# Performance work log

Measured on AMD Instinct MI355X. Metric: run time of the kernel, lower is better.

## Reference

```python
import jax, jax.numpy as jnp
import numpy as np


def setup_inputs() -> dict:
    key = jax.random.key(0)
    ks = jax.random.split(key, 8)
    C, dk = 256, 32
    B, H, W = 4, 64, 64
    x = jax.random.normal(ks[0], (B, C, H, W), dtype=jnp.float32)
    wq = jax.random.normal(ks[1], (dk, C), dtype=jnp.float32) * (1.0 / np.sqrt(C))
    bq = jnp.zeros((dk,), dtype=jnp.float32)
    wk = jax.random.normal(ks[2], (dk, C), dtype=jnp.float32) * (1.0 / np.sqrt(C))
    bk = jnp.zeros((dk,), dtype=jnp.float32)
    wv = jax.random.normal(ks[3], (C, C), dtype=jnp.float32) * (1.0 / np.sqrt(C))
    bv = jnp.zeros((C,), dtype=jnp.float32)
    gamma = jnp.ones((1,), dtype=jnp.float32)
    return {"x": x, "wq": wq, "bq": bq, "wk": wk, "bk": bk,
            "wv": wv, "bv": bv, "gamma": gamma}


def reference(x, wq, bq, wk, bk, wv, bv, gamma):
    B, C, H, W = x.shape
    N = H * W
    xf = x.reshape(B, C, N)  # [B, C, N]
    # 1x1 convs == per-pixel linear projections
    q = jnp.einsum('dc,bcn->bnd', wq, xf) + bq  # [B, N, dk]  (proj_query, permuted)
    k = jnp.einsum('dc,bcn->bdn', wk, xf) + bk[None, :, None]  # [B, dk, N]
    v = jnp.einsum('ec,bcn->ben', wv, xf) + bv[None, :, None]  # [B, C, N]
    energy = jnp.einsum('bnd,bdm->bnm', q, k)  # [B, N, N]
    attention = jax.nn.softmax(energy, axis=-1)
    # out[b,c,i] = sum_j v[b,c,j] * attention[b,i,j]
    out = jnp.einsum('bcj,bij->bci', v, attention)  # [B, C, N]
    out = out.reshape(B, C, H, W)
    return gamma[0] * out + x
```

## Files before the change

kernel.cpp:

```cpp
#include <hip/hip_runtime.h>
#include <hip/hip_bf16.h>

#define NPIX 4096
#define CIN  256
#define DK   32

typedef __attribute__((ext_vector_type(8))) short short8;
typedef __attribute__((ext_vector_type(16))) float f32x16;

__device__ __forceinline__ unsigned short f2bf(float f) {
    unsigned int u = __float_as_uint(f);
    return (unsigned short)((u + 0x7fffu + ((u >> 16) & 1u)) >> 16);
}
__device__ __forceinline__ float bf2f(unsigned short h) {
    return __uint_as_float(((unsigned int)h) << 16);
}
__device__ __forceinline__ unsigned int f2bf2(float a, float b) {
    __hip_bfloat162 h = __float22bfloat162_rn(make_float2(a, b));
    unsigned int u;
    __builtin_memcpy(&u, &h, 4);
    return u;
}

__global__ void wprep_kernel(const float* __restrict__ wq, const float* __restrict__ wk,
                             const float* __restrict__ wv,
                             unsigned short* __restrict__ wqh, unsigned short* __restrict__ wql,
                             unsigned short* __restrict__ wkh, unsigned short* __restrict__ wkl,
                             unsigned short* __restrict__ wvh) {
    const int lane = threadIdx.x & 63, li = lane & 31, hi = lane >> 5;
    const int kc = blockIdx.x, y = blockIdx.y;
    if (y < 4) {
        const float* m = (y < 2) ? wq : wk;
        short8 h8, l8;
#pragma unroll
        for (int e = 0; e < 8; ++e) {
            float v = m[li * CIN + kc * 16 + hi * 8 + e];
            unsigned short hb = f2bf(v);
            h8[e] = (short)hb;
            l8[e] = (short)f2bf(v - bf2f(hb));
        }
        unsigned short* dst = (y == 0) ? wqh : (y == 1) ? wql : (y == 2) ? wkh : wkl;
        *reinterpret_cast<short8*>(&dst[kc * 512 + lane * 8]) = (y & 1) ? l8 : h8;
    } else {
        const int cblk = y - 4;
        short8 h8;
#pragma unroll
        for (int e = 0; e < 8; ++e)
            h8[e] = (short)f2bf(wv[(cblk * 32 + li) * CIN + kc * 16 + hi * 8 + e]);
        *reinterpret_cast<short8*>(&wvh[(cblk * 16 + kc) * 512 + lane * 8]) = h8;
    }
}

__global__ __launch_bounds__(512) void projall_kernel(
        const float* __restrict__ x,
        const unsigned short* __restrict__ wqh, const unsigned short* __restrict__ wql,
        const unsigned short* __restrict__ wkh, const unsigned short* __restrict__ wkl,
        const unsigned short* __restrict__ wvh,
        const float* __restrict__ bq, const float* __restrict__ bk, const float* __restrict__ bv,
        unsigned short* __restrict__ qfrag, unsigned short* __restrict__ kfrag,
        unsigned short* __restrict__ vfrag) {
    __shared__ float xs[64][36];
    __shared__ unsigned short xhf[16 * 512];
    __shared__ unsigned short xlf[16 * 512];
    __shared__ unsigned short ts[2][32][40];

    const int t = threadIdx.x, lane = t & 63, li = lane & 31, hi = lane >> 5, w = t >> 6;
    const int nblk = blockIdx.x, b = blockIdx.y;
    const int n0 = nblk * 32;

    for (int cb = 0; cb < 4; ++cb) {
        {
            int c = t >> 3, n4 = (t & 7) * 4;
            float4 v = *reinterpret_cast<const float4*>(
                &x[(size_t)(b * CIN + cb * 64 + c) * NPIX + n0 + n4]);
            xs[c][n4 + 0] = v.x; xs[c][n4 + 1] = v.y;
            xs[c][n4 + 2] = v.z; xs[c][n4 + 3] = v.w;
        }
        __syncthreads();
        {
            const int kc = w & 3;
            const bool isL = (w >= 4);
            short8 f;
#pragma unroll
            for (int e = 0; e < 8; ++e) {
                float v = xs[kc * 16 + hi * 8 + e][li];
                unsigned short hb = f2bf(v);
                f[e] = isL ? (short)f2bf(v - bf2f(hb)) : (short)hb;
            }
            unsigned short* dst = isL ? xlf : xhf;
            *reinterpret_cast<short8*>(&dst[(cb * 4 + kc) * 512 + lane * 8]) = f;
        }
        __syncthreads();
    }

    if (w < 2) {
        const unsigned short* wh = (w == 0) ? wqh : wkh;
        const unsigned short* wl = (w == 0) ? wql : wkl;
        const float* bias = (w == 0) ? bq : bk;
        f32x16 acc;
#pragma unroll
        for (int r = 0; r < 16; ++r) acc[r] = 0.f;
        for (int kc = 0; kc < 16; ++kc) {
            short8 ah = *reinterpret_cast<const short8*>(&xhf[kc * 512 + lane * 8]);
            short8 al = *reinterpret_cast<const short8*>(&xlf[kc * 512 + lane * 8]);
            short8 whf = *reinterpret_cast<const short8*>(&wh[kc * 512 + lane * 8]);
            short8 wlf = *reinterpret_cast<const short8*>(&wl[kc * 512 + lane * 8]);
            acc = __builtin_amdgcn_mfma_f32_32x32x16_bf16(ah, whf, acc, 0, 0, 0);
            acc = __builtin_amdgcn_mfma_f32_32x32x16_bf16(al, whf, acc, 0, 0, 0);
            acc = __builtin_amdgcn_mfma_f32_32x32x16_bf16(ah, wlf, acc, 0, 0, 0);
        }
        const float bs = bias[li];
#pragma unroll
        for (int r = 0; r < 16; ++r) {
            int row = (r & 3) + 8 * (r >> 2) + 4 * hi;
            ts[w][row][li] = f2bf(acc[r] + bs);
        }
        unsigned short* dstf = (w == 0) ? qfrag : kfrag;
#pragma unroll
        for (int dh = 0; dh < 2; ++dh) {
            short8 f = *reinterpret_cast<const short8*>(&ts[w][li][dh * 16 + hi * 8]);
            *reinterpret_cast<short8*>(
                &dstf[((size_t)(b * 128 + nblk) * 2 + dh) * 512 + lane * 8]) = f;
        }
    } else {
        const int w2 = w - 2;
        const int njob = (w2 < 2) ? 2 : 1;
        for (int jj = 0; jj < njob; ++jj) {
            const int cblk = w2 + jj * 6;
            f32x16 acc;
#pragma unroll
            for (int r = 0; r < 16; ++r) acc[r] = 0.f;
            for (int kc = 0; kc < 16; ++kc) {
                short8 xb = *reinterpret_cast<const short8*>(&xhf[kc * 512 + lane * 8]);
                short8 wf = *reinterpret_cast<const short8*>(&wvh[(cblk * 16 + kc) * 512 + lane * 8]);
                acc = __builtin_amdgcn_mfma_f32_32x32x16_bf16(xb, wf, acc, 0, 0, 0);
            }
            const float bvv = bv[cblk * 32 + li];
#pragma unroll
            for (int g = 0; g < 2; ++g) {
                short8 sv;
#pragma unroll
                for (int e = 0; e < 8; ++e) sv[e] = (short)f2bf(acc[g * 8 + e] + bvv);
                *reinterpret_cast<short8*>(
                    &vfrag[((size_t)(b * 8 + cblk) * 256 + nblk * 2 + g) * 512 + lane * 8]) = sv;
            }
        }
    }
}

__global__ __launch_bounds__(512, 4) void attnv_kernel(
        const unsigned short* __restrict__ qfrag, const unsigned short* __restrict__ kfrag,
        const unsigned short* __restrict__ vfrag, unsigned short* __restrict__ opart,
        float* __restrict__ lpart, float* __restrict__ out) {
    __shared__ unsigned short Ps[4 * 8 * 512];
    __shared__ float sred[2][4][32];

    const int t = threadIdx.x, lane = t & 63, li = lane & 31, hi = lane >> 5, w = t >> 6;
    const int blk = blockIdx.x;
    const int xcd = blk & 7, slot = blk >> 3;
    const int jh = slot & 1, ps = slot >> 1;
    const int b = xcd >> 1;
    const int ipos = (xcd & 1) * 32 + ps;
    const int it = w >> 2, sl = w & 3;
    const int cq = w;

    short8 qb0, qb1;
    {
        size_t qoff = ((size_t)(b * 128 + ipos * 2 + it) * 2) * 512 + lane * 8;
        qb0 = *reinterpret_cast<const short8*>(&qfrag[qoff]);
        qb1 = *reinterpret_cast<const short8*>(&qfrag[qoff + 512]);
    }
    float ssum = 0.f;

    f32x16 acc0, acc1;
#pragma unroll
    for (int r = 0; r < 16; ++r) { acc0[r] = 0.f; acc1[r] = 0.f; }

    short8 kp0, kp1;
    short8 vp[8];

    auto kload = [&](int s) {
        size_t koff = ((size_t)(b * 128 + jh * 64 + s * 4 + sl) * 2) * 512 + lane * 8;
        kp0 = *reinterpret_cast<const short8*>(&kfrag[koff]);
        kp1 = *reinterpret_cast<const short8*>(&kfrag[koff + 512]);
    };
    auto vload = [&](int s) {
        size_t vb = ((size_t)(b * 8 + cq) * 256 + jh * 128 + s * 8) * 512 + lane * 8;
#pragma unroll
        for (int kc = 0; kc < 8; ++kc)
            vp[kc] = *reinterpret_cast<const short8*>(&vfrag[vb + kc * 512]);
    };
    auto do_E = [&](int s) {
        f32x16 e;
#pragma unroll
        for (int r = 0; r < 16; ++r) e[r] = 0.f;
        e = __builtin_amdgcn_mfma_f32_32x32x16_bf16(kp0, qb0, e, 0, 0, 0);
        e = __builtin_amdgcn_mfma_f32_32x32x16_bf16(kp1, qb1, e, 0, 0, 0);
        const int buf = s & 1;
#pragma unroll
        for (int g = 0; g < 2; ++g) {
            float p0 = __expf(e[g * 8 + 0]), p1 = __expf(e[g * 8 + 1]);
            float p2 = __expf(e[g * 8 + 2]), p3 = __expf(e[g * 8 + 3]);
            float p4 = __expf(e[g * 8 + 4]), p5 = __expf(e[g * 8 + 5]);
            float p6 = __expf(e[g * 8 + 6]), p7 = __expf(e[g * 8 + 7]);
            ssum += ((p0 + p1) + (p2 + p3)) + ((p4 + p5) + (p6 + p7));
            uint4 pk;
            pk.x = f2bf2(p0, p1); pk.y = f2bf2(p2, p3);
            pk.z = f2bf2(p4, p5); pk.w = f2bf2(p6, p7);
            *reinterpret_cast<uint4*>(
                &Ps[((it * 2 + buf) * 8 + sl * 2 + g) * 512 + lane * 8]) = pk;
        }
    };

    kload(0);
    vload(0);
    do_E(0);
    kload(1);
    __syncthreads();

#pragma unroll 1
    for (int s = 0; s < 16; ++s) {
        if (s + 1 < 16) {
            do_E(s + 1);
            if (s + 2 < 16) kload(s + 2);
        }
        const int buf = s & 1;
#pragma unroll
        for (int kc = 0; kc < 8; ++kc) {
            short8 B0 = *reinterpret_cast<const short8*>(&Ps[(buf * 8 + kc) * 512 + lane * 8]);
            short8 B1 = *reinterpret_cast<const short8*>(&Ps[((2 + buf) * 8 + kc) * 512 + lane * 8]);
            acc0 = __builtin_amdgcn_mfma_f32_32x32x16_bf16(vp[kc], B0, acc0, 0, 0, 0);
            acc1 = __builtin_amdgcn_mfma_f32_32x32x16_bf16(vp[kc], B1, acc1, 0, 0, 0);
        }
        if (s + 1 < 16) vload(s + 1);
        __syncthreads();
    }

    ssum += __shfl_xor(ssum, 32);
    if (lane < 32) sred[it][sl][li] = ssum;
    __syncthreads();
    if (sl == 0 && lane < 32) {
        float lt = sred[it][0][li] + sred[it][1][li] + sred[it][2][li] + sred[it][3][li];
        lpart[((size_t)jh * 4 + b) * NPIX + ipos * 64 + it * 32 + li] = lt;
    }

#pragma unroll
    for (int itt = 0; itt < 2; ++itt) {
        const f32x16& A = itt ? acc1 : acc0;
#pragma unroll
        for (int r = 0; r < 16; ++r) {
            int c = cq * 32 + (r & 3) + 8 * (r >> 2) + 4 * hi;
            size_t idx = (size_t)(b * CIN + c) * NPIX + ipos * 64 + itt * 32 + li;
            if (jh == 0) out[idx] = A[r];
            else         opart[idx] = f2bf(A[r]);
        }
    }
}

__global__ __launch_bounds__(256) void merge_kernel(
        const unsigned short* __restrict__ opart, const float* __restrict__ lpart,
        const float* __restrict__ xin, const float* __restrict__ gamma,
        float* __restrict__ out) {
    const size_t idx4 = ((size_t)blockIdx.x * 256 + threadIdx.x) * 4;
    const size_t i  = idx4 & (NPIX - 1);
    const size_t b  = idx4 >> 20;
    float4 o0 = *reinterpret_cast<const float4*>(&out[idx4]);
    float4 xv = *reinterpret_cast<const float4*>(&xin[idx4]);
    float4 l0 = *reinterpret_cast<const float4*>(&lpart[b * NPIX + i]);
    float4 l1 = *reinterpret_cast<const float4*>(&lpart[(4 + b) * NPIX + i]);
    const unsigned short* op = &opart[idx4];
    const float g = gamma[0];
    float4 o;
    o.x = g * (o0.x + bf2f(op[0])) / (l0.x + l1.x) + xv.x;
    o.y = g * (o0.y + bf2f(op[1])) / (l0.y + l1.y) + xv.y;
    o.z = g * (o0.z + bf2f(op[2])) / (l0.z + l1.z) + xv.z;
    o.w = g * (o0.w + bf2f(op[3])) / (l0.w + l1.w) + xv.w;
    *reinterpret_cast<float4*>(&out[idx4]) = o;
}

extern "C" void kernel_launch(void* const* d_in, const int* in_sizes, int n_in,
                              void* d_out, int out_size, void* d_ws, size_t ws_size,
                              hipStream_t stream) {
    const float* x     = (const float*)d_in[0];
    const float* wq    = (const float*)d_in[1];
    const float* bq    = (const float*)d_in[2];
    const float* wk    = (const float*)d_in[3];
    const float* bk    = (const float*)d_in[4];
    const float* wv    = (const float*)d_in[5];
    const float* bv    = (const float*)d_in[6];
    const float* gamma = (const float*)d_in[7];
    float* out = (float*)d_out;

    unsigned short* qf    = (unsigned short*)d_ws;
    unsigned short* kf    = qf + (size_t)524288;
    unsigned short* vf    = kf + (size_t)524288;
    unsigned short* wqh   = vf + (size_t)4194304;
    unsigned short* wql   = wqh + 8192;
    unsigned short* wkh   = wql + 8192;
    unsigned short* wkl   = wkh + 8192;
    unsigned short* wvh   = wkl + 8192;
    unsigned short* opart = wvh + 65536;
    float*          lpart = (float*)(opart + 4194304);

    wprep_kernel<<<dim3(16, 12), 64, 0, stream>>>(wq, wk, wv, wqh, wql, wkh, wkl, wvh);
    projall_kernel<<<dim3(128, 4), 512, 0, stream>>>(x, wqh, wql, wkh, wkl, wvh,
                                                     bq, bk, bv, qf, kf, vf);
    attnv_kernel<<<dim3(512), 512, 0, stream>>>(qf, kf, vf, opart, lpart, out);
    merge_kernel<<<dim3(4096), 256, 0, stream>>>(opart, lpart, x, gamma, out);
}
```

Before: 143.1 us.

## Specialize warps into producer (QK+exp) and consumer (PV MFMA) roles

Splits the 8 waves of the attention kernel into four producer waves that compute QK^T energies, exponentiate, and write bf16 probabilities to shared memory, and four consumer waves that each run the PV MFMAs for two channel groups. The aim is to overlap exp/VALU work with MFMA work across waves instead of serializing them within each wave. In exchange, consumer waves hold twice as many accumulators, which raises register pressure, and the V loads are interleaved in a rolling prefetch. Barrier counts must still match between the two roles.

```diff
diff --git a/kernel.cpp b/kernel.cpp
--- a/kernel.cpp
+++ b/kernel.cpp
@@ -161,98 +161,133 @@
     const int jh = slot & 1, ps = slot >> 1;
     const int b = xcd >> 1;
     const int ipos = (xcd & 1) * 32 + ps;
-    const int it = w >> 2, sl = w & 3;
-    const int cq = w;
-
-    short8 qb0, qb1;
-    {
-        size_t qoff = ((size_t)(b * 128 + ipos * 2 + it) * 2) * 512 + lane * 8;
-        qb0 = *reinterpret_cast<const short8*>(&qfrag[qoff]);
-        qb1 = *reinterpret_cast<const short8*>(&qfrag[qoff + 512]);
-    }
-    float ssum = 0.f;
-
-    f32x16 acc0, acc1;
-#pragma unroll
-    for (int r = 0; r < 16; ++r) { acc0[r] = 0.f; acc1[r] = 0.f; }
-
-    short8 kp0, kp1;
-    short8 vp[8];
-
-    auto kload = [&](int s) {
-        size_t koff = ((size_t)(b * 128 + jh * 64 + s * 4 + sl) * 2) * 512 + lane * 8;
-        kp0 = *reinterpret_cast<const short8*>(&kfrag[koff]);
-        kp1 = *reinterpret_cast<const short8*>(&kfrag[koff + 512]);
-    };
-    auto vload = [&](int s) {
-        size_t vb = ((size_t)(b * 8 + cq) * 256 + jh * 128 + s * 8) * 512 + lane * 8;
+
+    if (w < 4) {
+        const int sl = w;
+        short8 qb00, qb01, qb10, qb11;
+        {
+            size_t q0 = ((size_t)(b * 128 + ipos * 2 + 0) * 2) * 512 + lane * 8;
+            size_t q1 = ((size_t)(b * 128 + ipos * 2 + 1) * 2) * 512 + lane * 8;
+            qb00 = *reinterpret_cast<const short8*>(&qfrag[q0]);
+            qb01 = *reinterpret_cast<const short8*>(&qfrag[q0 + 512]);
+            qb10 = *reinterpret_cast<const short8*>(&qfrag[q1]);
+            qb11 = *reinterpret_cast<const short8*>(&qfrag[q1 + 512]);
+        }
+        float ssum0 = 0.f, ssum1 = 0.f;
+        short8 kp0, kp1;
+
+        auto kload = [&](int s) {
+            size_t koff = ((size_t)(b * 128 + jh * 64 + s * 4 + sl) * 2) * 512 + lane * 8;
+            kp0 = *reinterpret_cast<const short8*>(&kfrag[koff]);
+            kp1 = *reinterpret_cast<const short8*>(&kfrag[koff + 512]);
+        };
+        auto eunit = [&](short8 qA, short8 qB, float& ss, int slab, int buf) {
+            f32x16 e;
+#pragma unroll
+            for (int r = 0; r < 16; ++r) e[r] = 0.f;
+            e = __builtin_amdgcn_mfma_f32_32x32x16_bf16(kp0, qA, e, 0, 0, 0);
+            e = __builtin_amdgcn_mfma_f32_32x32x16_bf16(kp1, qB, e, 0, 0, 0);
+#pragma unroll
+            for (int g = 0; g < 2; ++g) {
+                float p0 = __expf(e[g * 8 + 0]), p1 = __expf(e[g * 8 + 1]);
+                float p2 = __expf(e[g * 8 + 2]), p3 = __expf(e[g * 8 + 3]);
+                float p4 = __expf(e[g * 8 + 4]), p5 = __expf(e[g * 8 + 5]);
+                float p6 = __expf(e[g * 8 + 6]), p7 = __expf(e[g * 8 + 7]);
+                ss += ((p0 + p1) + (p2 + p3)) + ((p4 + p5) + (p6 + p7));
+                uint4 pk;
+                pk.x = f2bf2(p0, p1); pk.y = f2bf2(p2, p3);
+                pk.z = f2bf2(p4, p5); pk.w = f2bf2(p6, p7);
+                *reinterpret_cast<uint4*>(
+                    &Ps[((slab + buf) * 8 + sl * 2 + g) * 512 + lane * 8]) = pk;
+            }
+        };
+        auto do_E2 = [&](int s) {
+            const int buf = s & 1;
+            eunit(qb00, qb01, ssum0, 0, buf);
+            eunit(qb10, qb11, ssum1, 2, buf);
+        };
+
+        kload(0);
+        do_E2(0);
+        kload(1);
+        __syncthreads();
+#pragma unroll 1
+        for (int s = 0; s < 16; ++s) {
+            if (s + 1 < 16) {
+                do_E2(s + 1);
+                if (s + 2 < 16) kload(s + 2);
+            }
+            __syncthreads();
+        }
+
+        ssum0 += __shfl_xor(ssum0, 32);
+        ssum1 += __shfl_xor(ssum1, 32);
+        if (lane < 32) { sred[0][sl][li] = ssum0; sred[1][sl][li] = ssum1; }
+        __syncthreads();
+        if (w < 2 && lane < 32) {
+            float lt = sred[w][0][li] + sred[w][1][li] + sred[w][2][li] + sred[w][3][li];
+            lpart[((size_t)jh * 4 + b) * NPIX + ipos * 64 + w * 32 + li] = lt;
+        }
+    } else {
+        const int cqa = w - 4, cqb = w;
+        f32x16 aA0, aA1, aB0, aB1;
+#pragma unroll
+        for (int r = 0; r < 16; ++r) { aA0[r] = 0.f; aA1[r] = 0.f; aB0[r] = 0.f; aB1[r] = 0.f; }
+
+        short8 vp[8];
+        const size_t vbA = ((size_t)(b * 8 + cqa) * 256 + jh * 128) * 512 + lane * 8;
+        const size_t vbB = ((size_t)(b * 8 + cqb) * 256 + jh * 128) * 512 + lane * 8;
+
 #pragma unroll
         for (int kc = 0; kc < 8; ++kc)
-            vp[kc] = *reinterpret_cast<const short8*>(&vfrag[vb + kc * 512]);
-    };
-    auto do_E = [&](int s) {
-        f32x16 e;
-#pragma unroll
-        for (int r = 0; r < 16; ++r) e[r] = 0.f;
-        e = __builtin_amdgcn_mfma_f32_32x32x16_bf16(kp0, qb0, e, 0, 0, 0);
-        e = __builtin_amdgcn_mfma_f32_32x32x16_bf16(kp1, qb1, e, 0, 0, 0);
-        const int buf = s & 1;
-#pragma unroll
-        for (int g = 0; g < 2; ++g) {
-            float p0 = __expf(e[g * 8 + 0]), p1 = __expf(e[g * 8 + 1]);
-            float p2 = __expf(e[g * 8 + 2]), p3 = __expf(e[g * 8 + 3]);
-            float p4 = __expf(e[g * 8 + 4]), p5 = __expf(e[g * 8 + 5]);
-            float p6 = __expf(e[g * 8 + 6]), p7 = __expf(e[g * 8 + 7]);
-            ssum += ((p0 + p1) + (p2 + p3)) + ((p4 + p5) + (p6 + p7));
-            uint4 pk;
-            pk.x = f2bf2(p0, p1); pk.y = f2bf2(p2, p3);
-            pk.z = f2bf2(p4, p5); pk.w = f2bf2(p6, p7);
-            *reinterpret_cast<uint4*>(
-                &Ps[((it * 2 + buf) * 8 + sl * 2 + g) * 512 + lane * 8]) = pk;
-        }
-    };
-
-    kload(0);
-    vload(0);
-    do_E(0);
-    kload(1);
-    __syncthreads();
+            vp[kc] = *reinterpret_cast<const short8*>(&vfrag[vbA + kc * 512]);
+        __syncthreads();
 
 #pragma unroll 1
-    for (int s = 0; s < 16; ++s) {
-        if (s + 1 < 16) {
-            do_E(s + 1);
-            if (s + 2 < 16) kload(s + 2);
-        }
-        const int buf = s & 1;
-#pragma unroll
-        for (int kc = 0; kc < 8; ++kc) {
-            short8 B0 = *reinterpret_cast<const short8*>(&Ps[(buf * 8 + kc) * 512 + lane * 8]);
-            short8 B1 = *reinterpret_cast<const short8*>(&Ps[((2 + buf) * 8 + kc) * 512 + lane * 8]);
-            acc0 = __builtin_amdgcn_mfma_f32_32x32x16_bf16(vp[kc], B0, acc0, 0, 0, 0);
-            acc1 = __builtin_amdgcn_mfma_f32_32x32x16_bf16(vp[kc], B1, acc1, 0, 0, 0);
-        }
-        if (s + 1 < 16) vload(s + 1);
-        __syncthreads();
-    }
-
-    ssum += __shfl_xor(ssum, 32);
-    if (lane < 32) sred[it][sl][li] = ssum;
-    __syncthreads();
-    if (sl == 0 && lane < 32) {
-        float lt = sred[it][0][li] + sred[it][1][li] + sred[it][2][li] + sred[it][3][li];
-        lpart[((size_t)jh * 4 + b) * NPIX + ipos * 64 + it * 32 + li] = lt;
-    }
-
-#pragma unroll
-    for (int itt = 0; itt < 2; ++itt) {
-        const f32x16& A = itt ? acc1 : acc0;
-#pragma unroll
-        for (int r = 0; r < 16; ++r) {
-            int c = cq * 32 + (r & 3) + 8 * (r >> 2) + 4 * hi;
-            size_t idx = (size_t)(b * CIN + c) * NPIX + ipos * 64 + itt * 32 + li;
-            if (jh == 0) out[idx] = A[r];
-            else         opart[idx] = f2bf(A[r]);
+        for (int s = 0; s < 16; ++s) {
+            const int buf = s & 1;
+            {
+                const size_t pB = vbB + (size_t)s * 8 * 512;
+#pragma unroll
+                for (int kc = 0; kc < 8; ++kc) {
+                    short8 a = vp[kc];
+                    vp[kc] = *reinterpret_cast<const short8*>(&vfrag[pB + kc * 512]);
+                    short8 B0 = *reinterpret_cast<const short8*>(&Ps[(buf * 8 + kc) * 512 + lane * 8]);
+                    short8 B1 = *reinterpret_cast<const short8*>(&Ps[((2 + buf) * 8 + kc) * 512 + lane * 8]);
+                    aA0 = __builtin_amdgcn_mfma_f32_32x32x16_bf16(a, B0, aA0, 0, 0, 0);
+                    aA1 = __builtin_amdgcn_mfma_f32_32x32x16_bf16(a, B1, aA1, 0, 0, 0);
+                }
+            }
+            {
+                const size_t pA = vbA + (size_t)(s + 1) * 8 * 512;
+#pragma unroll
+                for (int kc = 0; kc < 8; ++kc) {
+                    short8 a = vp[kc];
+                    vp[kc] = *reinterpret_cast<const short8*>(&vfrag[pA + kc * 512]);
+                    short8 B0 = *reinterpret_cast<const short8*>(&Ps[(buf * 8 + kc) * 512 + lane * 8]);
+                    short8 B1 = *reinterpret_cast<const short8*>(&Ps[((2 + buf) * 8 + kc) * 512 + lane * 8]);
+                    aB0 = __builtin_amdgcn_mfma_f32_32x32x16_bf16(a, B0, aB0, 0, 0, 0);
+                    aB1 = __builtin_amdgcn_mfma_f32_32x32x16_bf16(a, B1, aB1, 0, 0, 0);
+                }
+            }
+            __syncthreads();
+        }
+        __syncthreads();
+
+#pragma unroll
+        for (int cqi = 0; cqi < 2; ++cqi) {
+            const int cq = cqi ? cqb : cqa;
+#pragma unroll
+            for (int itt = 0; itt < 2; ++itt) {
+                const f32x16 A = cqi ? (itt ? aB1 : aB0) : (itt ? aA1 : aA0);
+#pragma unroll
+                for (int r = 0; r < 16; ++r) {
+                    int c = cq * 32 + (r & 3) + 8 * (r >> 2) + 4 * hi;
+                    size_t idx = (size_t)(b * CIN + c) * NPIX + ipos * 64 + itt * 32 + li;
+                    if (jh == 0) out[idx] = A[r];
+                    else         opart[idx] = f2bf(A[r]);
+                }
+            }
         }
     }
 }
```

Result: slower. 148.9 us (+4.1%).
